# Kernel optimization log

Measured on AMD Instinct MI355X. Metric: run time of the kernel, lower is better.

The kernel has to match this reference:

```python
import jax, jax.numpy as jnp
import numpy as np

N_QUBITS = 4
DEPTH = 3
OUT_DIM = 256
BN_EPS = 1e-5


def _apply_ry(state, theta, q):
    # state: (B,2,2,2,2) complex64, theta: (B,) float32, gate on qubit q
    st = jnp.moveaxis(state, q + 1, -1)            # (B,2,2,2,2) with target last
    half = theta * 0.5
    c = jnp.cos(half)[:, None, None, None]
    s = jnp.sin(half)[:, None, None, None]
    a0, a1 = st[..., 0], st[..., 1]
    st = jnp.stack([c * a0 - s * a1, s * a0 + c * a1], axis=-1)
    return jnp.moveaxis(st, -1, q + 1)


def _apply_rz(state, theta, q):
    # theta: scalar (shared param). RZ = diag(e^{-i t/2}, e^{i t/2})
    st = jnp.moveaxis(state, q + 1, -1)
    p0 = jnp.exp(-0.5j * theta)
    p1 = jnp.exp(0.5j * theta)
    st = jnp.stack([st[..., 0] * p0, st[..., 1] * p1], axis=-1)
    return jnp.moveaxis(st, -1, q + 1)


def _apply_cnot(state, c, t):
    st = jnp.moveaxis(state, (c + 1, t + 1), (-2, -1))  # (...,2_c,2_t)
    st = jnp.stack([st[..., 0, :], st[..., 1, ::-1]], axis=-2)
    return jnp.moveaxis(st, (-2, -1), (c + 1, t + 1))


def _simulate(qparams, x):
    # Batched 4-qubit statevector sim. x: (B,4) data angles, qparams: (24,)
    B = x.shape[0]
    state = jnp.zeros((B, 16), jnp.complex64).at[:, 0].set(1.0)
    state = state.reshape(B, 2, 2, 2, 2)
    for d in range(DEPTH):
        for i in range(N_QUBITS):
            # RY(data) then RY(param) on same wire == RY(data+param)
            state = _apply_ry(state, x[:, i] + qparams[d * 2 * N_QUBITS + i], i)
        for i in range(N_QUBITS):
            state = _apply_cnot(state, i, (i + 1) % N_QUBITS)
        for i in range(N_QUBITS):
            theta = qparams[d * 2 * N_QUBITS + N_QUBITS + i]
            state = _apply_rz(state, jnp.broadcast_to(theta, ()), i)
    probs = jnp.abs(state) ** 2                      # (B,2,2,2,2) float32
    axes = (1, 2, 3, 4)
    z = []
    for i in range(N_QUBITS):
        p = probs.sum(axis=tuple(a for a in axes if a != i + 1))  # (B,2)
        z.append(p[:, 0] - p[:, 1])
    return jnp.stack(z, axis=1).astype(jnp.float32)  # (B,4) <Z_i>


def _batchnorm(h, g, b):
    m = h.mean(axis=0)
    v = h.var(axis=0)  # biased, as torch uses for normalization in train mode
    return (h - m) * jax.lax.rsqrt(v + BN_EPS) * g + b


def setup_inputs() -> dict:
    key = jax.random.key(0)
    ks = jax.random.split(key, 8)
    B = 65536
    x = jax.random.normal(ks[0], (B, N_QUBITS), jnp.float32)
    qparams = jax.random.normal(ks[1], (DEPTH * 2 * N_QUBITS,), jnp.float32)
    fc1_w = jax.random.normal(ks[2], (128, N_QUBITS), jnp.float32) * 0.3
    fc1_b = jnp.zeros((128,), jnp.float32)
    fc2_w = jax.random.normal(ks[3], (256, 128), jnp.float32) * 0.08
    fc2_b = jnp.zeros((256,), jnp.float32)
    fc3_w = jax.random.normal(ks[4], (OUT_DIM, 256), jnp.float32) * 0.06
    fc3_b = jnp.zeros((OUT_DIM,), jnp.float32)
    bn1_g = jnp.ones((128,), jnp.float32)
    bn1_b = jnp.zeros((128,), jnp.float32)
    bn2_g = jnp.ones((256,), jnp.float32)
    bn2_b = jnp.zeros((256,), jnp.float32)
    return dict(x=x, qparams=qparams, fc1_w=fc1_w, fc1_b=fc1_b,
                bn1_g=bn1_g, bn1_b=bn1_b, fc2_w=fc2_w, fc2_b=fc2_b,
                bn2_g=bn2_g, bn2_b=bn2_b, fc3_w=fc3_w, fc3_b=fc3_b)


def reference(x, qparams, fc1_w, fc1_b, bn1_g, bn1_b, fc2_w, fc2_b,
              bn2_g, bn2_b, fc3_w, fc3_b):
    q = _simulate(qparams, x)                              # (B,4)
    h = jax.nn.relu(_batchnorm(q @ fc1_w.T + fc1_b, bn1_g, bn1_b))
    h = jax.nn.relu(_batchnorm(h @ fc2_w.T + fc2_b, bn2_g, bn2_b))
    out = jnp.tanh(h @ fc3_w.T + fc3_b)                    # (B,256)
    return out.reshape(-1, 1, 16, 16)
```

## Files before the change

kernel.cpp:

```cpp
#include <hip/hip_runtime.h>

typedef __attribute__((ext_vector_type(8))) _Float16 f16x8;
typedef __attribute__((ext_vector_type(16))) float f32x16;

#define MFMA32(a, b, c) __builtin_amdgcn_mfma_f32_32x32x16_f16((a), (b), (c), 0, 0, 0)

__device__ __forceinline__ float tanh_fast(float x) {
  return 1.0f - 2.0f / (__expf(2.0f * x) + 1.0f);
}

__global__ __launch_bounds__(256) void k_quantum(
    const float4* __restrict__ x, const float* __restrict__ qp,
    float4* __restrict__ qout, float* __restrict__ s1part, int QB,
    const float* __restrict__ w2, const float* __restrict__ w3,
    _Float16* __restrict__ w2f, _Float16* __restrict__ w3f,
    float* __restrict__ s2sum, float* __restrict__ s2sq)
{
  int tid = threadIdx.x;

  if (blockIdx.x >= QB) {
    int tb = blockIdx.x - QB;
    int i = tb * 256 + tid;
    w3f[i] = (_Float16)w3[i];
    if (i < 32768) w2f[i] = (_Float16)w2[i];
    if (tb == 0) { s2sum[tid] = 0.f; s2sq[tid] = 0.f; }
    return;
  }

  size_t r = (size_t)blockIdx.x * 256 + tid;
  float4 xr = x[r];
  float xv[4] = {xr.x, xr.y, xr.z, xr.w};

  float re[16], im[16];
#pragma unroll
  for (int i = 0; i < 16; i++) { re[i] = 0.f; im[i] = 0.f; }
  re[0] = 1.f;

#pragma unroll
  for (int d = 0; d < 3; d++) {
#pragma unroll
    for (int q = 0; q < 4; q++) {
      float th = 0.5f * (xv[q] + qp[d * 8 + q]);
      float s, c; __sincosf(th, &s, &c);
      int m = 8 >> q;
#pragma unroll
      for (int i = 0; i < 16; i++) if (!(i & m)) {
        int i1 = i | m;
        float r0 = re[i], i0 = im[i], r1 = re[i1], i1v = im[i1];
        re[i]  = c * r0 - s * r1;  im[i]  = c * i0 - s * i1v;
        re[i1] = s * r0 + c * r1;  im[i1] = s * i0 + c * i1v;
      }
    }
#pragma unroll
    for (int q = 0; q < 4; q++) {
      int mc = 8 >> q, mt = 8 >> ((q + 1) & 3);
#pragma unroll
      for (int i = 0; i < 16; i++) if ((i & mc) && !(i & mt)) {
        int i1 = i | mt;
        float tr = re[i]; re[i] = re[i1]; re[i1] = tr;
        float ti = im[i]; im[i] = im[i1]; im[i1] = ti;
      }
    }
#pragma unroll
    for (int q = 0; q < 4; q++) {
      float th = 0.5f * qp[d * 8 + 4 + q];
      float s, c; __sincosf(th, &s, &c);
      int m = 8 >> q;
#pragma unroll
      for (int i = 0; i < 16; i++) {
        float pi = (i & m) ? s : -s;
        float r0 = re[i], i0 = im[i];
        re[i] = r0 * c - i0 * pi;
        im[i] = r0 * pi + i0 * c;
      }
    }
  }

  float p[16];
#pragma unroll
  for (int i = 0; i < 16; i++) p[i] = re[i] * re[i] + im[i] * im[i];
  float z[4];
#pragma unroll
  for (int q = 0; q < 4; q++) {
    int m = 8 >> q; float acc = 0.f;
#pragma unroll
    for (int i = 0; i < 16; i++) acc += (i & m) ? -p[i] : p[i];
    z[q] = acc;
  }
  qout[r] = make_float4(z[0], z[1], z[2], z[3]);

  float st[14];
  st[0] = z[0]; st[1] = z[1]; st[2] = z[2]; st[3] = z[3];
  int p5 = 4;
#pragma unroll
  for (int a = 0; a < 4; a++)
#pragma unroll
    for (int b = a; b < 4; b++) st[p5++] = z[a] * z[b];

  __shared__ float part[4][14];
  int lane = tid & 63, wv = tid >> 6;
#pragma unroll
  for (int s = 0; s < 14; s++) {
    float v = st[s];
#pragma unroll
    for (int o = 32; o; o >>= 1) v += __shfl_down(v, o, 64);
    if (lane == 0) part[wv][s] = v;
  }
  __syncthreads();
  if (tid < 14)
    s1part[blockIdx.x * 14 + tid] =
        part[0][tid] + part[1][tid] + part[2][tid] + part[3][tid];
}

__global__ __launch_bounds__(256, 2) void k_fc2stats(
    const float4* __restrict__ q, const float* __restrict__ s1part, int QB,
    const float* __restrict__ w1p, const float* __restrict__ b1p,
    const float* __restrict__ g1p, const float* __restrict__ bb1p,
    const _Float16* __restrict__ w2f, const float* __restrict__ b2,
    float* __restrict__ s2sum, float* __restrict__ s2sq, float invB)
{
  __shared__ __align__(16) float4 qs[128];
  __shared__ __align__(16) _Float16 a1[128 * 136];
  __shared__ float r1[14][16];
  __shared__ float s1v[14];
  __shared__ __align__(16) float4 w1eS[128];
  __shared__ float b1eS[128];

  int t = threadIdx.x;
  int lane = t & 63, w = t >> 6, m32 = lane & 31, hh = lane >> 5;
  size_t rowBase = (size_t)blockIdx.x * 128;

  if (t < 128) qs[t] = q[rowBase + t];
  if (t < 224) {
    int s = t >> 4, k = t & 15;
    float acc = 0.f;
    for (int j = k; j < QB; j += 16) acc += s1part[j * 14 + s];
    r1[s][k] = acc;
  }
  __syncthreads();
  if (t < 14) {
    float v = 0.f;
#pragma unroll
    for (int k = 0; k < 16; k++) v += r1[t][k];
    s1v[t] = v * invB;
  }
  __syncthreads();

  if (t < 128) {
    int j = t;
    float S0 = s1v[0], S1 = s1v[1], S2 = s1v[2], S3 = s1v[3];
    float M00 = s1v[4], M01 = s1v[5], M02 = s1v[6], M03 = s1v[7];
    float M11 = s1v[8], M12 = s1v[9], M13 = s1v[10];
    float M22 = s1v[11], M23 = s1v[12], M33 = s1v[13];
    float w0 = w1p[j * 4 + 0], wv1 = w1p[j * 4 + 1], wv2 = w1p[j * 4 + 2], wv3 = w1p[j * 4 + 3];
    float b = b1p[j];
    float wq = w0 * S0 + wv1 * S1 + wv2 * S2 + wv3 * S3;
    float mm = wq + b;
    float quad = w0 * w0 * M00 + wv1 * wv1 * M11 + wv2 * wv2 * M22 + wv3 * wv3 * M33
               + 2.f * (w0 * wv1 * M01 + w0 * wv2 * M02 + w0 * wv3 * M03
                      + wv1 * wv2 * M12 + wv1 * wv3 * M13 + wv2 * wv3 * M23);
    float e2 = quad + 2.f * b * wq + b * b;
    float var = e2 - mm * mm;
    float sv = g1p[j] * rsqrtf(var + 1e-5f);
    w1eS[j] = make_float4(sv * w0, sv * wv1, sv * wv2, sv * wv3);
    b1eS[j] = sv * b + bb1p[j] - sv * mm;
  }
  __syncthreads();

  {
    int j = t & 127;
    float4 w1v = w1eS[j];
    float b1v = b1eS[j];
    int rb = (t >> 7) * 64;
#pragma unroll 8
    for (int i = 0; i < 64; i++) {
      float4 qv = qs[rb + i];
      float v = fmaf(w1v.x, qv.x, fmaf(w1v.y, qv.y, fmaf(w1v.z, qv.z, fmaf(w1v.w, qv.w, b1v))));
      a1[(rb + i) * 136 + j] = (_Float16)fmaxf(v, 0.f);
    }
  }
  __syncthreads();

  f32x16 acc[4][2];
#pragma unroll
  for (int mt = 0; mt < 4; mt++)
#pragma unroll
    for (int nt = 0; nt < 2; nt++)
#pragma unroll
      for (int r = 0; r < 16; r++) acc[mt][nt][r] = 0.f;

#pragma unroll
  for (int ks = 0; ks < 8; ks++) {
    int kb = ks * 16 + hh * 8;
    f16x8 bfr[2];
#pragma unroll
    for (int nt = 0; nt < 2; nt++)
      bfr[nt] = *(const f16x8*)(w2f + (size_t)(w * 64 + nt * 32 + m32) * 128 + kb);
#pragma unroll
    for (int mt = 0; mt < 4; mt++) {
      f16x8 afr = *(const f16x8*)&a1[(mt * 32 + m32) * 136 + kb];
#pragma unroll
      for (int nt = 0; nt < 2; nt++)
        acc[mt][nt] = MFMA32(afr, bfr[nt], acc[mt][nt]);
    }
  }

#pragma unroll
  for (int nt = 0; nt < 2; nt++) {
    int col = w * 64 + nt * 32 + m32;
    float b2v = b2[col];
    float s = 0.f, ss = 0.f;
#pragma unroll
    for (int mt = 0; mt < 4; mt++)
#pragma unroll
      for (int r = 0; r < 16; r++) {
        float hv = acc[mt][nt][r] + b2v;
        s += hv; ss += hv * hv;
      }
    s += __shfl_down(s, 32, 64);
    ss += __shfl_down(ss, 32, 64);
    if (lane < 32) {
      atomicAdd(&s2sum[col], s);
      atomicAdd(&s2sq[col], ss);
    }
  }
}

__global__ __launch_bounds__(256, 2) void k_final(
    const float4* __restrict__ q, const float* __restrict__ s1part, int QB,
    const float* __restrict__ w1p, const float* __restrict__ b1p,
    const float* __restrict__ g1p, const float* __restrict__ bb1p,
    const _Float16* __restrict__ w2f, const float* __restrict__ b2,
    const float* __restrict__ g2p, const float* __restrict__ bb2p,
    const float* __restrict__ s2sum, const float* __restrict__ s2sq,
    const _Float16* __restrict__ w3f, const float* __restrict__ b3,
    float* __restrict__ out, float invB)
{
  __shared__ __align__(16) float4 qs[128];
  __shared__ __align__(16) _Float16 un[128 * 264];
  __shared__ float r1[14][16];
  __shared__ float s1v[14];
  __shared__ __align__(16) float4 w1eS[128];
  __shared__ float b1eS[128];
  __shared__ float sc2s[256];
  __shared__ float t2s[256];

  int t = threadIdx.x;
  int lane = t & 63, w = t >> 6, m32 = lane & 31, hh = lane >> 5;
  size_t rowBase = (size_t)blockIdx.x * 128;

  if (t < 128) qs[t] = q[rowBase + t];
  if (t < 224) {
    int s = t >> 4, k = t & 15;
    float acc = 0.f;
    for (int j = k; j < QB; j += 16) acc += s1part[j * 14 + s];
    r1[s][k] = acc;
  }
  {
    float mcol = s2sum[t] * invB;
    float vcol = s2sq[t] * invB - mcol * mcol;
    float sv = g2p[t] * rsqrtf(vcol + 1e-5f);
    sc2s[t] = sv;
    t2s[t] = bb2p[t] - mcol * sv + b2[t] * sv;
  }
  __syncthreads();
  if (t < 14) {
    float v = 0.f;
#pragma unroll
    for (int k = 0; k < 16; k++) v += r1[t][k];
    s1v[t] = v * invB;
  }
  __syncthreads();

  if (t < 128) {
    int j = t;
    float S0 = s1v[0], S1 = s1v[1], S2 = s1v[2], S3 = s1v[3];
    float M00 = s1v[4], M01 = s1v[5], M02 = s1v[6], M03 = s1v[7];
    float M11 = s1v[8], M12 = s1v[9], M13 = s1v[10];
    float M22 = s1v[11], M23 = s1v[12], M33 = s1v[13];
    float w0 = w1p[j * 4 + 0], wv1 = w1p[j * 4 + 1], wv2 = w1p[j * 4 + 2], wv3 = w1p[j * 4 + 3];
    float b = b1p[j];
    float wq = w0 * S0 + wv1 * S1 + wv2 * S2 + wv3 * S3;
    float mm = wq + b;
    float quad = w0 * w0 * M00 + wv1 * wv1 * M11 + wv2 * wv2 * M22 + wv3 * wv3 * M33
               + 2.f * (w0 * wv1 * M01 + w0 * wv2 * M02 + w0 * wv3 * M03
                      + wv1 * wv2 * M12 + wv1 * wv3 * M13 + wv2 * wv3 * M23);
    float e2 = quad + 2.f * b * wq + b * b;
    float var = e2 - mm * mm;
    float sv = g1p[j] * rsqrtf(var + 1e-5f);
    w1eS[j] = make_float4(sv * w0, sv * wv1, sv * wv2, sv * wv3);
    b1eS[j] = sv * b + bb1p[j] - sv * mm;
  }
  __syncthreads();

  {
    int j = t & 127;
    float4 w1v = w1eS[j];
    float b1v = b1eS[j];
    int rb = (t >> 7) * 64;
#pragma unroll 8
    for (int i = 0; i < 64; i++) {
      float4 qv = qs[rb + i];
      float v = fmaf(w1v.x, qv.x, fmaf(w1v.y, qv.y, fmaf(w1v.z, qv.z, fmaf(w1v.w, qv.w, b1v))));
      un[(rb + i) * 136 + j] = (_Float16)fmaxf(v, 0.f);
    }
  }
  __syncthreads();

  f32x16 acc[4][2];
#pragma unroll
  for (int mt = 0; mt < 4; mt++)
#pragma unroll
    for (int nt = 0; nt < 2; nt++)
#pragma unroll
      for (int r = 0; r < 16; r++) acc[mt][nt][r] = 0.f;

#pragma unroll
  for (int ks = 0; ks < 8; ks++) {
    int kb = ks * 16 + hh * 8;
    f16x8 bfr[2];
#pragma unroll
    for (int nt = 0; nt < 2; nt++)
      bfr[nt] = *(const f16x8*)(w2f + (size_t)(w * 64 + nt * 32 + m32) * 128 + kb);
#pragma unroll
    for (int mt = 0; mt < 4; mt++) {
      f16x8 afr = *(const f16x8*)&un[(mt * 32 + m32) * 136 + kb];
#pragma unroll
      for (int nt = 0; nt < 2; nt++)
        acc[mt][nt] = MFMA32(afr, bfr[nt], acc[mt][nt]);
    }
  }
  __syncthreads();

#pragma unroll
  for (int nt = 0; nt < 2; nt++) {
    int col = w * 64 + nt * 32 + m32;
    float sv = sc2s[col], tv = t2s[col];
#pragma unroll
    for (int mt = 0; mt < 4; mt++)
#pragma unroll
      for (int r = 0; r < 16; r++) {
        int row = mt * 32 + (r & 3) + 8 * (r >> 2) + 4 * hh;
        un[row * 264 + col] = (_Float16)fmaxf(fmaf(acc[mt][nt][r], sv, tv), 0.f);
      }
  }
  __syncthreads();

  f32x16 acc3[4][2];
#pragma unroll
  for (int mt = 0; mt < 4; mt++)
#pragma unroll
    for (int nt = 0; nt < 2; nt++)
#pragma unroll
      for (int r = 0; r < 16; r++) acc3[mt][nt][r] = 0.f;

#pragma unroll
  for (int ks = 0; ks < 16; ks++) {
    int kb = ks * 16 + hh * 8;
    f16x8 bfr[2];
#pragma unroll
    for (int nt = 0; nt < 2; nt++)
      bfr[nt] = *(const f16x8*)(w3f + (size_t)(w * 64 + nt * 32 + m32) * 256 + kb);
#pragma unroll
    for (int mt = 0; mt < 4; mt++) {
      f16x8 afr = *(const f16x8*)&un[(mt * 32 + m32) * 264 + kb];
#pragma unroll
      for (int nt = 0; nt < 2; nt++)
        acc3[mt][nt] = MFMA32(afr, bfr[nt], acc3[mt][nt]);
    }
  }

#pragma unroll
  for (int nt = 0; nt < 2; nt++) {
    int col = w * 64 + nt * 32 + m32;
    float b3v = b3[col];
#pragma unroll
    for (int mt = 0; mt < 4; mt++)
#pragma unroll
      for (int r = 0; r < 16; r++) {
        int row = mt * 32 + (r & 3) + 8 * (r >> 2) + 4 * hh;
        out[(rowBase + row) * 256 + col] = tanh_fast(acc3[mt][nt][r] + b3v);
      }
  }
}

extern "C" void kernel_launch(void* const* d_in, const int* in_sizes, int n_in,
                              void* d_out, int out_size, void* d_ws, size_t ws_size,
                              hipStream_t stream) {
  const float* x     = (const float*)d_in[0];
  const float* qp    = (const float*)d_in[1];
  const float* fc1_w = (const float*)d_in[2];
  const float* fc1_b = (const float*)d_in[3];
  const float* bn1_g = (const float*)d_in[4];
  const float* bn1_b = (const float*)d_in[5];
  const float* fc2_w = (const float*)d_in[6];
  const float* fc2_b = (const float*)d_in[7];
  const float* bn2_g = (const float*)d_in[8];
  const float* bn2_b = (const float*)d_in[9];
  const float* fc3_w = (const float*)d_in[10];
  const float* fc3_b = (const float*)d_in[11];
  float* out = (float*)d_out;
  float* ws  = (float*)d_ws;

  int B = in_sizes[0] / 4;
  int QB = B / 256;
  float invB = 1.0f / (float)B;

  float* wq     = ws;
  float* s1part = ws + (size_t)4 * B;
  float* s2sum  = s1part + (size_t)QB * 14;
  float* s2sq   = s2sum + 256;
  _Float16* w2f = (_Float16*)(s2sq + 256);
  _Float16* w3f = w2f + 32768;

  k_quantum<<<QB + 256, 256, 0, stream>>>((const float4*)x, qp, (float4*)wq, s1part, QB,
                                          fc2_w, fc3_w, w2f, w3f, s2sum, s2sq);
  k_fc2stats<<<B / 128, 256, 0, stream>>>((const float4*)wq, s1part, QB,
                                          fc1_w, fc1_b, bn1_g, bn1_b,
                                          w2f, fc2_b, s2sum, s2sq, invB);
  k_final<<<B / 128, 256, 0, stream>>>((const float4*)wq, s1part, QB,
                                       fc1_w, fc1_b, bn1_g, bn1_b,
                                       w2f, fc2_b, bn2_g, bn2_b,
                                       s2sum, s2sq, w3f, fc3_b, out, invB);
}
```

Baseline: 146.4 us.

## Double threads per block in FC kernels, one N-tile per wave

```diff
diff --git a/kernel.cpp b/kernel.cpp
--- a/kernel.cpp
+++ b/kernel.cpp
@@ -112,7 +112,7 @@
         part[0][tid] + part[1][tid] + part[2][tid] + part[3][tid];
 }
 
-__global__ __launch_bounds__(256, 2) void k_fc2stats(
+__global__ __launch_bounds__(512, 4) void k_fc2stats(
     const float4* __restrict__ q, const float* __restrict__ s1part, int QB,
     const float* __restrict__ w1p, const float* __restrict__ b1p,
     const float* __restrict__ g1p, const float* __restrict__ bb1p,
@@ -121,7 +121,7 @@
 {
   __shared__ __align__(16) float4 qs[128];
   __shared__ __align__(16) _Float16 a1[128 * 136];
-  __shared__ float r1[14][16];
+  __shared__ float r1[14][32];
   __shared__ float s1v[14];
   __shared__ __align__(16) float4 w1eS[128];
   __shared__ float b1eS[128];
@@ -131,17 +131,17 @@
   size_t rowBase = (size_t)blockIdx.x * 128;
 
   if (t < 128) qs[t] = q[rowBase + t];
-  if (t < 224) {
-    int s = t >> 4, k = t & 15;
+  if (t < 448) {
+    int s = t >> 5, k = t & 31;
     float acc = 0.f;
-    for (int j = k; j < QB; j += 16) acc += s1part[j * 14 + s];
+    for (int j = k; j < QB; j += 32) acc += s1part[j * 14 + s];
     r1[s][k] = acc;
   }
   __syncthreads();
   if (t < 14) {
     float v = 0.f;
 #pragma unroll
-    for (int k = 0; k < 16; k++) v += r1[t][k];
+    for (int k = 0; k < 32; k++) v += r1[t][k];
     s1v[t] = v * invB;
   }
   __syncthreads();
@@ -171,9 +171,9 @@
     int j = t & 127;
     float4 w1v = w1eS[j];
     float b1v = b1eS[j];
-    int rb = (t >> 7) * 64;
+    int rb = (t >> 7) * 32;
 #pragma unroll 8
-    for (int i = 0; i < 64; i++) {
+    for (int i = 0; i < 32; i++) {
       float4 qv = qs[rb + i];
       float v = fmaf(w1v.x, qv.x, fmaf(w1v.y, qv.y, fmaf(w1v.z, qv.z, fmaf(w1v.w, qv.w, b1v))));
       a1[(rb + i) * 136 + j] = (_Float16)fmaxf(v, 0.f);
@@ -181,40 +181,32 @@
   }
   __syncthreads();
 
-  f32x16 acc[4][2];
+  f32x16 acc[4];
 #pragma unroll
   for (int mt = 0; mt < 4; mt++)
 #pragma unroll
-    for (int nt = 0; nt < 2; nt++)
-#pragma unroll
-      for (int r = 0; r < 16; r++) acc[mt][nt][r] = 0.f;
-
+    for (int r = 0; r < 16; r++) acc[mt][r] = 0.f;
+
+  int col = w * 32 + m32;
 #pragma unroll
   for (int ks = 0; ks < 8; ks++) {
     int kb = ks * 16 + hh * 8;
-    f16x8 bfr[2];
-#pragma unroll
-    for (int nt = 0; nt < 2; nt++)
-      bfr[nt] = *(const f16x8*)(w2f + (size_t)(w * 64 + nt * 32 + m32) * 128 + kb);
+    f16x8 bfr = *(const f16x8*)(w2f + (size_t)col * 128 + kb);
 #pragma unroll
     for (int mt = 0; mt < 4; mt++) {
       f16x8 afr = *(const f16x8*)&a1[(mt * 32 + m32) * 136 + kb];
-#pragma unroll
-      for (int nt = 0; nt < 2; nt++)
-        acc[mt][nt] = MFMA32(afr, bfr[nt], acc[mt][nt]);
-    }
-  }
-
-#pragma unroll
-  for (int nt = 0; nt < 2; nt++) {
-    int col = w * 64 + nt * 32 + m32;
+      acc[mt] = MFMA32(afr, bfr, acc[mt]);
+    }
+  }
+
+  {
     float b2v = b2[col];
     float s = 0.f, ss = 0.f;
 #pragma unroll
     for (int mt = 0; mt < 4; mt++)
 #pragma unroll
       for (int r = 0; r < 16; r++) {
-        float hv = acc[mt][nt][r] + b2v;
+        float hv = acc[mt][r] + b2v;
         s += hv; ss += hv * hv;
       }
     s += __shfl_down(s, 32, 64);
@@ -226,7 +218,7 @@
   }
 }
 
-__global__ __launch_bounds__(256, 2) void k_final(
+__global__ __launch_bounds__(512, 4) void k_final(
     const float4* __restrict__ q, const float* __restrict__ s1part, int QB,
     const float* __restrict__ w1p, const float* __restrict__ b1p,
     const float* __restrict__ g1p, const float* __restrict__ bb1p,
@@ -238,7 +230,7 @@
 {
   __shared__ __align__(16) float4 qs[128];
   __shared__ __align__(16) _Float16 un[128 * 264];
-  __shared__ float r1[14][16];
+  __shared__ float r1[14][32];
   __shared__ float s1v[14];
   __shared__ __align__(16) float4 w1eS[128];
   __shared__ float b1eS[128];
@@ -250,13 +242,13 @@
   size_t rowBase = (size_t)blockIdx.x * 128;
 
   if (t < 128) qs[t] = q[rowBase + t];
-  if (t < 224) {
-    int s = t >> 4, k = t & 15;
+  if (t < 448) {
+    int s = t >> 5, k = t & 31;
     float acc = 0.f;
-    for (int j = k; j < QB; j += 16) acc += s1part[j * 14 + s];
+    for (int j = k; j < QB; j += 32) acc += s1part[j * 14 + s];
     r1[s][k] = acc;
   }
-  {
+  if (t < 256) {
     float mcol = s2sum[t] * invB;
     float vcol = s2sq[t] * invB - mcol * mcol;
     float sv = g2p[t] * rsqrtf(vcol + 1e-5f);
@@ -267,7 +259,7 @@
   if (t < 14) {
     float v = 0.f;
 #pragma unroll
-    for (int k = 0; k < 16; k++) v += r1[t][k];
+    for (int k = 0; k < 32; k++) v += r1[t][k];
     s1v[t] = v * invB;
   }
   __syncthreads();
@@ -297,9 +289,9 @@
     int j = t & 127;
     float4 w1v = w1eS[j];
     float b1v = b1eS[j];
-    int rb = (t >> 7) * 64;
+    int rb = (t >> 7) * 32;
 #pragma unroll 8
-    for (int i = 0; i < 64; i++) {
+    for (int i = 0; i < 32; i++) {
       float4 qv = qs[rb + i];
       float v = fmaf(w1v.x, qv.x, fmaf(w1v.y, qv.y, fmaf(w1v.z, qv.z, fmaf(w1v.w, qv.w, b1v))));
       un[(rb + i) * 136 + j] = (_Float16)fmaxf(v, 0.f);
@@ -307,79 +299,62 @@
   }
   __syncthreads();
 
-  f32x16 acc[4][2];
+  int col = w * 32 + m32;
+  f32x16 acc[4];
 #pragma unroll
   for (int mt = 0; mt < 4; mt++)
 #pragma unroll
-    for (int nt = 0; nt < 2; nt++)
-#pragma unroll
-      for (int r = 0; r < 16; r++) acc[mt][nt][r] = 0.f;
+    for (int r = 0; r < 16; r++) acc[mt][r] = 0.f;
 
 #pragma unroll
   for (int ks = 0; ks < 8; ks++) {
     int kb = ks * 16 + hh * 8;
-    f16x8 bfr[2];
-#pragma unroll
-    for (int nt = 0; nt < 2; nt++)
-      bfr[nt] = *(const f16x8*)(w2f + (size_t)(w * 64 + nt * 32 + m32) * 128 + kb);
+    f16x8 bfr = *(const f16x8*)(w2f + (size_t)col * 128 + kb);
 #pragma unroll
     for (int mt = 0; mt < 4; mt++) {
       f16x8 afr = *(const f16x8*)&un[(mt * 32 + m32) * 136 + kb];
-#pragma unroll
-      for (int nt = 0; nt < 2; nt++)
-        acc[mt][nt] = MFMA32(afr, bfr[nt], acc[mt][nt]);
-    }
-  }
-  __syncthreads();
-
-#pragma unroll
-  for (int nt = 0; nt < 2; nt++) {
-    int col = w * 64 + nt * 32 + m32;
+      acc[mt] = MFMA32(afr, bfr, acc[mt]);
+    }
+  }
+  __syncthreads();
+
+  {
     float sv = sc2s[col], tv = t2s[col];
 #pragma unroll
     for (int mt = 0; mt < 4; mt++)
 #pragma unroll
       for (int r = 0; r < 16; r++) {
         int row = mt * 32 + (r & 3) + 8 * (r >> 2) + 4 * hh;
-        un[row * 264 + col] = (_Float16)fmaxf(fmaf(acc[mt][nt][r], sv, tv), 0.f);
-      }
-  }
-  __syncthreads();
-
-  f32x16 acc3[4][2];
+        un[row * 264 + col] = (_Float16)fmaxf(fmaf(acc[mt][r], sv, tv), 0.f);
+      }
+  }
+  __syncthreads();
+
+  f32x16 acc3[4];
 #pragma unroll
   for (int mt = 0; mt < 4; mt++)
 #pragma unroll
-    for (int nt = 0; nt < 2; nt++)
-#pragma unroll
-      for (int r = 0; r < 16; r++) acc3[mt][nt][r] = 0.f;
+    for (int r = 0; r < 16; r++) acc3[mt][r] = 0.f;
 
 #pragma unroll
   for (int ks = 0; ks < 16; ks++) {
     int kb = ks * 16 + hh * 8;
-    f16x8 bfr[2];
-#pragma unroll
-    for (int nt = 0; nt < 2; nt++)
-      bfr[nt] = *(const f16x8*)(w3f + (size_t)(w * 64 + nt * 32 + m32) * 256 + kb);
+    f16x8 bfr = *(const f16x8*)(w3f + (size_t)col * 256 + kb);
 #pragma unroll
     for (int mt = 0; mt < 4; mt++) {
       f16x8 afr = *(const f16x8*)&un[(mt * 32 + m32) * 264 + kb];
-#pragma unroll
-      for (int nt = 0; nt < 2; nt++)
-        acc3[mt][nt] = MFMA32(afr, bfr[nt], acc3[mt][nt]);
-    }
-  }
-
-#pragma unroll
-  for (int nt = 0; nt < 2; nt++) {
-    int col = w * 64 + nt * 32 + m32;
+      acc3[mt] = MFMA32(afr, bfr, acc3[mt]);
+    }
+  }
+
+  {
     float b3v = b3[col];
 #pragma unroll
     for (int mt = 0; mt < 4; mt++)
 #pragma unroll
       for (int r = 0; r < 16; r++) {
         int row = mt * 32 + (r & 3) + 8 * (r >> 2) + 4 * hh;
-        out[(rowBase + row) * 256 + col] = tanh_fast(acc3[mt][nt][r] + b3v);
+        out[(rowBase + row) * 256 + col] = tanh_fast(acc3[mt][r] + b3v);
       }
   }
 }
@@ -415,10 +390,10 @@
 
   k_quantum<<<QB + 256, 256, 0, stream>>>((const float4*)x, qp, (float4*)wq, s1part, QB,
                                           fc2_w, fc3_w, w2f, w3f, s2sum, s2sq);
-  k_fc2stats<<<B / 128, 256, 0, stream>>>((const float4*)wq, s1part, QB,
+  k_fc2stats<<<B / 128, 512, 0, stream>>>((const float4*)wq, s1part, QB,
                                           fc1_w, fc1_b, bn1_g, bn1_b,
                                           w2f, fc2_b, s2sum, s2sq, invB);
-  k_final<<<B / 128, 256, 0, stream>>>((const float4*)wq, s1part, QB,
+  k_final<<<B / 128, 512, 0, stream>>>((const float4*)wq, s1part, QB,
                                        fc1_w, fc1_b, bn1_g, bn1_b,
                                        w2f, fc2_b, bn2_g, bn2_b,
                                        s2sum, s2sq, w3f, fc3_b, out, invB);
```

Measured after the change: 146.1 us. No clear change (-0.2%).
